# Performance work log

Measured on AMD Instinct MI355X. Metric: run time of the kernel, lower is better.

## Reference

```python
import jax, jax.numpy as jnp
import numpy as np

B, T, D_IN, D_H, D_OUT = 32, 1024, 512, 1024, 512

def setup_inputs() -> dict:
    key = jax.random.key(0)
    kx, k1, k2, k3, k4, k5, k6 = jax.random.split(key, 7)
    # scale weights like typical init (1/sqrt(fan_in)) so sigmoid stays in a sane range
    x = jax.random.normal(kx, (B, T, D_IN), dtype=jnp.float32)
    Wh_w = jax.random.normal(k1, (D_H, D_H), dtype=jnp.float32) / np.sqrt(D_H)
    Wh_b = jax.random.normal(k2, (D_H,), dtype=jnp.float32) * 0.01
    Wx_w = jax.random.normal(k3, (D_H, D_IN), dtype=jnp.float32) / np.sqrt(D_IN)
    Wx_b = jax.random.normal(k4, (D_H,), dtype=jnp.float32) * 0.01
    Wy_w = jax.random.normal(k5, (D_OUT, D_H), dtype=jnp.float32) / np.sqrt(D_H)
    Wy_b = jax.random.normal(k6, (D_OUT,), dtype=jnp.float32) * 0.01
    return {"x": x, "Wh_w": Wh_w, "Wh_b": Wh_b, "Wx_w": Wx_w, "Wx_b": Wx_b,
            "Wy_w": Wy_w, "Wy_b": Wy_b}

def reference(x, Wh_w, Wh_b, Wx_w, Wx_b, Wy_w, Wy_b):
    # h_t = sigmoid(Wh h_{t-1} + b_h + Wx x_t + b_x); y_t = Wy h_t + b_y
    # Precompute input projection for all timesteps (one big GEMM).
    xp = jnp.einsum('bti,hi->bth', x, Wx_w) + Wx_b + Wh_b  # [B,T,H]
    xp_t = jnp.swapaxes(xp, 0, 1)  # [T,B,H] for scan
    h0 = jnp.zeros((x.shape[0], Wh_w.shape[0]), dtype=x.dtype)

    def step(h, xpt):
        h = jax.nn.sigmoid(h @ Wh_w.T + xpt)  # [B,H]
        y = h @ Wy_w.T + Wy_b                 # [B,O]
        return h, y

    _, ys = jax.lax.scan(step, h0, xp_t)  # ys: [T,B,O]
    return jnp.swapaxes(ys, 0, 1)  # [B,T,O]
```

## Files before the change

kernel.cpp:

```cpp
#include <hip/hip_runtime.h>

constexpr int Bb = 32;
constexpr int Tt = 1024;
constexpr int Hh = 1024;
constexpr int Di = 512;
constexpr int Do = 512;
constexpr int TGSZ = Bb * Hh;

using bf16x8 = __attribute__((ext_vector_type(8))) short;
using f32x4  = __attribute__((ext_vector_type(4))) float;

__device__ __forceinline__ f32x4 mfma16(bf16x8 a, bf16x8 b, f32x4 c) {
  return __builtin_amdgcn_mfma_f32_16x16x32_bf16(a, b, c, 0, 0, 0);
}
__device__ __forceinline__ unsigned short f2bf(float f) {
  unsigned u = __builtin_bit_cast(unsigned, f);
  u += 0x7FFFu + ((u >> 16) & 1u);
  return (unsigned short)(u >> 16);
}
__device__ __forceinline__ float bf2f(unsigned short h) {
  unsigned u = ((unsigned)h) << 16;
  return __builtin_bit_cast(float, u);
}

__global__ __launch_bounds__(256) void cvt4_kernel(const float* __restrict__ s,
                                                   unsigned short* __restrict__ d) {
  int i = (blockIdx.x * 256 + threadIdx.x) * 4;
  float4 v = *(const float4*)(s + i);
  ushort4 u = { f2bf(v.x), f2bf(v.y), f2bf(v.z), f2bf(v.w) };
  *(ushort4*)(d + i) = u;
}

__global__ __launch_bounds__(256) void init_tags(unsigned* __restrict__ tg) {
  int i = blockIdx.x * 256 + threadIdx.x;
  tg[i] = (i < TGSZ) ? 0xFFFF0000u : 0xEEEE0000u;
}

template <int MODE>
__global__ __launch_bounds__(256)
void gemm_kernel(const void* __restrict__ Ap, const float* __restrict__ Bw,
                 const float* __restrict__ bias1, const float* __restrict__ bias2,
                 void* __restrict__ Cp) {
  constexpr int K = (MODE == 0) ? Di : Hh;
  constexpr int BM = 64, BN = 64, BK = 64;
  __shared__ unsigned short As[BM][80];
  __shared__ unsigned short Bs[BN][80];

  const int m0 = blockIdx.x * BM;
  const int n0 = blockIdx.y * BN;
  const int tid = threadIdx.x;
  const int lane = tid & 63;
  const int wave = tid >> 6;
  const int wm = (wave & 1) * 32;
  const int wn = (wave >> 1) * 32;
  const int fr = lane & 15;
  const int kg = lane >> 4;

  f32x4 acc[2][2] = {};

  const int srow = tid >> 2;
  const int scb  = (tid & 3) * 16;

  for (int k0 = 0; k0 < K; k0 += BK) {
    if constexpr (MODE == 0) {
      const float* a = (const float*)Ap + (size_t)(m0 + srow) * K + k0 + scb;
#pragma unroll
      for (int q = 0; q < 4; ++q) {
        float4 v = ((const float4*)a)[q];
        ushort4 u = { f2bf(v.x), f2bf(v.y), f2bf(v.z), f2bf(v.w) };
        *(ushort4*)&As[srow][scb + q * 4] = u;
      }
    } else {
      const unsigned short* a = (const unsigned short*)Ap + (size_t)(m0 + srow) * K + k0 + scb;
      *(uint4*)&As[srow][scb]     = ((const uint4*)a)[0];
      *(uint4*)&As[srow][scb + 8] = ((const uint4*)a)[1];
    }
    {
      const float* b = Bw + (size_t)(n0 + srow) * K + k0 + scb;
#pragma unroll
      for (int q = 0; q < 4; ++q) {
        float4 v = ((const float4*)b)[q];
        ushort4 u = { f2bf(v.x), f2bf(v.y), f2bf(v.z), f2bf(v.w) };
        *(ushort4*)&Bs[srow][scb + q * 4] = u;
      }
    }
    __syncthreads();

#pragma unroll
    for (int kk = 0; kk < 2; ++kk) {
      const int kb = kk * 32 + kg * 8;
      bf16x8 af[2], bfr[2];
      af[0]  = *(const bf16x8*)&As[wm + fr][kb];
      af[1]  = *(const bf16x8*)&As[wm + 16 + fr][kb];
      bfr[0] = *(const bf16x8*)&Bs[wn + fr][kb];
      bfr[1] = *(const bf16x8*)&Bs[wn + 16 + fr][kb];
#pragma unroll
      for (int i = 0; i < 2; ++i)
#pragma unroll
        for (int j = 0; j < 2; ++j)
          acc[i][j] = mfma16(af[i], bfr[j], acc[i][j]);
    }
    __syncthreads();
  }

#pragma unroll
  for (int i = 0; i < 2; ++i) {
#pragma unroll
    for (int j = 0; j < 2; ++j) {
      const int n = n0 + wn + j * 16 + fr;
      float bv;
      if constexpr (MODE == 0) bv = bias1[n] + bias2[n];
      else                     bv = bias1[n];
#pragma unroll
      for (int q = 0; q < 4; ++q) {
        const int m = m0 + wm + i * 16 + kg * 4 + q;
        float v = acc[i][j][q] + bv;
        if constexpr (MODE == 0) {
          int bb = m >> 10, ttt = m & 1023;
          ((unsigned short*)Cp)[((size_t)ttt * Bb + bb) * Hh + n] = f2bf(v);
        } else {
          int bb = m & 31, ttt = m >> 5;
          ((float*)Cp)[((size_t)bb * Tt + ttt) * Do + n] = v;
        }
      }
    }
  }
}

__global__ __launch_bounds__(512, 2)
void scan_kernel(const unsigned short* __restrict__ Whb,
                 const unsigned short* __restrict__ xp,
                 unsigned short* __restrict__ hist,
                 unsigned* __restrict__ tg) {
  __shared__ unsigned short panel[16 * 1024];

  const int tid = threadIdx.x;
  const int g = blockIdx.x >> 3;
  const int r = blockIdx.x & 7;
  const int wave = tid >> 6;
  const int lane = tid & 63;
  const int nloc = lane & 15;
  const int kgrp = lane >> 4;
  const int hrow = r * 128 + wave * 16 + nloc;
  const int gb0 = g * 16;
  const int xmask = (nloc & 7) << 3;

  bf16x8 wf[32];
  {
    const unsigned short* wb = Whb + (size_t)hrow * Hh + kgrp * 8;
#pragma unroll
    for (int kk = 0; kk < 32; kk += 8) {
      const unsigned short* p = wb + kk * 32;
      asm volatile(
          "global_load_dwordx4 %0, %8, off\n\t"
          "global_load_dwordx4 %1, %8, off offset:64\n\t"
          "global_load_dwordx4 %2, %8, off offset:128\n\t"
          "global_load_dwordx4 %3, %8, off offset:192\n\t"
          "global_load_dwordx4 %4, %8, off offset:256\n\t"
          "global_load_dwordx4 %5, %8, off offset:320\n\t"
          "global_load_dwordx4 %6, %8, off offset:384\n\t"
          "global_load_dwordx4 %7, %8, off offset:448\n\t"
          "s_waitcnt vmcnt(0)"
          : "=&v"(wf[kk + 0]), "=&v"(wf[kk + 1]), "=&v"(wf[kk + 2]), "=&v"(wf[kk + 3]),
            "=&v"(wf[kk + 4]), "=&v"(wf[kk + 5]), "=&v"(wf[kk + 6]), "=&v"(wf[kk + 7])
          : "v"(p)
          : "memory");
    }
  }

  const int sb  = tid & 15;
  const int kc  = tid >> 4;
  const int sxs = (sb & 7) << 3;

  for (int t = 0; t < Tt; ++t) {
    const int par = t % 3;
    const int nxt = (t + 1) % 3;

    unsigned short xpv[4];
    const size_t xb = (size_t)t * Bb * Hh + hrow;
#pragma unroll
    for (int i = 0; i < 4; ++i) xpv[i] = xp[xb + (size_t)(gb0 + kgrp * 4 + i) * Hh];

    const unsigned exp = ((unsigned)t - 1u) & 0xFFFFu;
    const unsigned* src = tg + (size_t)par * TGSZ + (size_t)(gb0 + sb) * Hh + kc * 32;
    uint4 d0, d1, d2, d3, d4, d5, d6, d7;
    unsigned bad;
    int tries = 8192;
    do {
      asm volatile(
          "global_load_dwordx4 %0, %8, off sc0 sc1\n\t"
          "global_load_dwordx4 %1, %8, off offset:16 sc0 sc1\n\t"
          "global_load_dwordx4 %2, %8, off offset:32 sc0 sc1\n\t"
          "global_load_dwordx4 %3, %8, off offset:48 sc0 sc1\n\t"
          "global_load_dwordx4 %4, %8, off offset:64 sc0 sc1\n\t"
          "global_load_dwordx4 %5, %8, off offset:80 sc0 sc1\n\t"
          "global_load_dwordx4 %6, %8, off offset:96 sc0 sc1\n\t"
          "global_load_dwordx4 %7, %8, off offset:112 sc0 sc1\n\t"
          "s_waitcnt vmcnt(0)"
          : "=&v"(d0), "=&v"(d1), "=&v"(d2), "=&v"(d3),
            "=&v"(d4), "=&v"(d5), "=&v"(d6), "=&v"(d7)
          : "v"(src) : "memory");
      bad = 0;
#define CHK(v) bad |= ((v.x >> 16) ^ exp) | ((v.y >> 16) ^ exp) | \
                      ((v.z >> 16) ^ exp) | ((v.w >> 16) ^ exp)
      CHK(d0); CHK(d1); CHK(d2); CHK(d3); CHK(d4); CHK(d5); CHK(d6); CHK(d7);
#undef CHK
    } while (bad && --tries);

    {
#define PK(a, b) (((a) & 0xFFFFu) | ((b) << 16))
      uint4 p0 = { PK(d0.x, d0.y), PK(d0.z, d0.w), PK(d1.x, d1.y), PK(d1.z, d1.w) };
      uint4 p1 = { PK(d2.x, d2.y), PK(d2.z, d2.w), PK(d3.x, d3.y), PK(d3.z, d3.w) };
      uint4 p2 = { PK(d4.x, d4.y), PK(d4.z, d4.w), PK(d5.x, d5.y), PK(d5.z, d5.w) };
      uint4 p3 = { PK(d6.x, d6.y), PK(d6.z, d6.w), PK(d7.x, d7.y), PK(d7.z, d7.w) };
#undef PK
      const int pb = sb * 1024, k0 = kc * 32;
      *(uint4*)&panel[pb + ((k0)      ^ sxs)] = p0;
      *(uint4*)&panel[pb + ((k0 + 8)  ^ sxs)] = p1;
      *(uint4*)&panel[pb + ((k0 + 16) ^ sxs)] = p2;
      *(uint4*)&panel[pb + ((k0 + 24) ^ sxs)] = p3;
    }
    __syncthreads();

    f32x4 acc0 = {0.f, 0.f, 0.f, 0.f}, acc1 = {0.f, 0.f, 0.f, 0.f};
#pragma unroll
    for (int kk = 0; kk < 32; kk += 2) {
      bf16x8 a0 = *(const bf16x8*)&panel[nloc * 1024 + ((kk * 32 + kgrp * 8) ^ xmask)];
      bf16x8 a1 = *(const bf16x8*)&panel[nloc * 1024 + (((kk + 1) * 32 + kgrp * 8) ^ xmask)];
      acc0 = mfma16(a0, wf[kk], acc0);
      acc1 = mfma16(a1, wf[kk + 1], acc1);
    }
    f32x4 acc = acc0 + acc1;

    const size_t tb = (size_t)t * Bb * Hh;
    unsigned* dbase = tg + (size_t)nxt * TGSZ + hrow;
#pragma unroll
    for (int i = 0; i < 4; ++i) {
      const int mb = gb0 + kgrp * 4 + i;
      float pre = acc[i] + bf2f(xpv[i]);
      float h = 1.0f / (1.0f + __expf(-pre));
      unsigned short hb = f2bf(h);
      unsigned word = ((unsigned)t << 16) | (unsigned)hb;
      asm volatile("global_store_dword %0, %1, off sc0 sc1"
                   :: "v"(dbase + (size_t)mb * Hh), "v"(word) : "memory");
      hist[tb + (size_t)mb * Hh + hrow] = hb;
    }

    __syncthreads();
  }
}

extern "C" void kernel_launch(void* const* d_in, const int* in_sizes, int n_in,
                              void* d_out, int out_size, void* d_ws, size_t ws_size,
                              hipStream_t stream) {
  const float* x    = (const float*)d_in[0];
  const float* Wh_w = (const float*)d_in[1];
  const float* Wh_b = (const float*)d_in[2];
  const float* Wx_w = (const float*)d_in[3];
  const float* Wx_b = (const float*)d_in[4];
  const float* Wy_w = (const float*)d_in[5];
  const float* Wy_b = (const float*)d_in[6];

  char* ws = (char*)d_ws;
  constexpr size_t XP_OFF   = 0;
  constexpr size_t HIST_OFF = XP_OFF   + (size_t)Tt * Bb * Hh * 2;
  constexpr size_t WH_OFF   = HIST_OFF + (size_t)Tt * Bb * Hh * 2;
  constexpr size_t TG_OFF   = WH_OFF   + (size_t)Hh * Hh * 2;

  unsigned short* xp   = (unsigned short*)(ws + XP_OFF);
  unsigned short* hist = (unsigned short*)(ws + HIST_OFF);
  unsigned short* whb  = (unsigned short*)(ws + WH_OFF);
  unsigned*       tg   = (unsigned*)(ws + TG_OFF);

  init_tags<<<dim3((3 * TGSZ) / 256), dim3(256), 0, stream>>>(tg);

  cvt4_kernel<<<dim3((Hh * Hh) / (256 * 4)), dim3(256), 0, stream>>>(Wh_w, whb);

  gemm_kernel<0><<<dim3((Bb * Tt) / 64, Hh / 64), dim3(256), 0, stream>>>(
      (const void*)x, Wx_w, Wx_b, Wh_b, (void*)xp);

  {
    void* sargs[4] = { (void*)&whb, (void*)&xp, (void*)&hist, (void*)&tg };
    hipLaunchCooperativeKernel((const void*)scan_kernel, dim3(16), dim3(512), sargs, 0, stream);
  }

  gemm_kernel<1><<<dim3((Bb * Tt) / 64, Do / 64), dim3(256), 0, stream>>>(
      (const void*)hist, Wy_w, Wy_b, nullptr, d_out);
}
```

Before: 5.856 ms.

## Replace tagged-word handoff with per-wave flags and direct global h loads

The scan's inter-block communication changes from 32-bit tagged words (value plus timestep), polled and repacked into LDS, to a double-buffered bf16 hidden-state array plus per-wave progress flags. Each wave polls 64 flags, then streams its A operand directly from global memory with pipelined loads interleaved with MFMAs, and needs no __syncthreads. The grid moves from 16 blocks of 512 threads to 32 blocks of 256, so more CUs take part. The aim is to halve handoff traffic and cut block-wide barriers from the per-step critical path, at the cost of redundant global reads of h per wave and a separate flag store after a full vmcnt wait.

```diff
diff --git a/kernel.cpp b/kernel.cpp
--- a/kernel.cpp
+++ b/kernel.cpp
@@ -5,7 +5,7 @@
 constexpr int Hh = 1024;
 constexpr int Di = 512;
 constexpr int Do = 512;
-constexpr int TGSZ = Bb * Hh;
+constexpr int BbHh = Bb * Hh;
 
 using bf16x8 = __attribute__((ext_vector_type(8))) short;
 using f32x4  = __attribute__((ext_vector_type(4))) float;
@@ -29,11 +29,6 @@
   float4 v = *(const float4*)(s + i);
   ushort4 u = { f2bf(v.x), f2bf(v.y), f2bf(v.z), f2bf(v.w) };
   *(ushort4*)(d + i) = u;
-}
-
-__global__ __launch_bounds__(256) void init_tags(unsigned* __restrict__ tg) {
-  int i = blockIdx.x * 256 + threadIdx.x;
-  tg[i] = (i < TGSZ) ? 0xFFFF0000u : 0xEEEE0000u;
 }
 
 template <int MODE>
@@ -127,23 +122,22 @@
   }
 }
 
-__global__ __launch_bounds__(512, 2)
+__global__ __launch_bounds__(256, 1)
 void scan_kernel(const unsigned short* __restrict__ Whb,
                  const unsigned short* __restrict__ xp,
                  unsigned short* __restrict__ hist,
-                 unsigned* __restrict__ tg) {
-  __shared__ unsigned short panel[16 * 1024];
-
+                 unsigned short* __restrict__ hbuf,
+                 unsigned* __restrict__ flags) {
   const int tid = threadIdx.x;
-  const int g = blockIdx.x >> 3;
-  const int r = blockIdx.x & 7;
+  const int g = blockIdx.x >> 4;
+  const int r = blockIdx.x & 15;
   const int wave = tid >> 6;
   const int lane = tid & 63;
   const int nloc = lane & 15;
   const int kgrp = lane >> 4;
-  const int hrow = r * 128 + wave * 16 + nloc;
+  const int W = r * 4 + wave;
+  const int hrow = W * 16 + nloc;
   const int gb0 = g * 16;
-  const int xmask = (nloc & 7) << 3;
 
   bf16x8 wf[32];
   {
@@ -168,85 +162,87 @@
     }
   }
 
-  const int sb  = tid & 15;
-  const int kc  = tid >> 4;
-  const int sxs = (sb & 7) << 3;
+  unsigned* fbase = flags + g * 64;
+  const unsigned* fp = fbase + lane;
 
   for (int t = 0; t < Tt; ++t) {
-    const int par = t % 3;
-    const int nxt = (t + 1) % 3;
+    const unsigned short* hrd = hbuf + (size_t)(t & 1) * BbHh;
+    unsigned short* hwr = hbuf + (size_t)((t + 1) & 1) * BbHh;
 
     unsigned short xpv[4];
-    const size_t xb = (size_t)t * Bb * Hh + hrow;
+    const size_t xb = (size_t)t * BbHh + hrow;
 #pragma unroll
     for (int i = 0; i < 4; ++i) xpv[i] = xp[xb + (size_t)(gb0 + kgrp * 4 + i) * Hh];
 
-    const unsigned exp = ((unsigned)t - 1u) & 0xFFFFu;
-    const unsigned* src = tg + (size_t)par * TGSZ + (size_t)(gb0 + sb) * Hh + kc * 32;
-    uint4 d0, d1, d2, d3, d4, d5, d6, d7;
-    unsigned bad;
-    int tries = 8192;
-    do {
-      asm volatile(
-          "global_load_dwordx4 %0, %8, off sc0 sc1\n\t"
-          "global_load_dwordx4 %1, %8, off offset:16 sc0 sc1\n\t"
-          "global_load_dwordx4 %2, %8, off offset:32 sc0 sc1\n\t"
-          "global_load_dwordx4 %3, %8, off offset:48 sc0 sc1\n\t"
-          "global_load_dwordx4 %4, %8, off offset:64 sc0 sc1\n\t"
-          "global_load_dwordx4 %5, %8, off offset:80 sc0 sc1\n\t"
-          "global_load_dwordx4 %6, %8, off offset:96 sc0 sc1\n\t"
-          "global_load_dwordx4 %7, %8, off offset:112 sc0 sc1\n\t"
-          "s_waitcnt vmcnt(0)"
-          : "=&v"(d0), "=&v"(d1), "=&v"(d2), "=&v"(d3),
-            "=&v"(d4), "=&v"(d5), "=&v"(d6), "=&v"(d7)
-          : "v"(src) : "memory");
-      bad = 0;
-#define CHK(v) bad |= ((v.x >> 16) ^ exp) | ((v.y >> 16) ^ exp) | \
-                      ((v.z >> 16) ^ exp) | ((v.w >> 16) ^ exp)
-      CHK(d0); CHK(d1); CHK(d2); CHK(d3); CHK(d4); CHK(d5); CHK(d6); CHK(d7);
-#undef CHK
-    } while (bad && --tries);
-
     {
-#define PK(a, b) (((a) & 0xFFFFu) | ((b) << 16))
-      uint4 p0 = { PK(d0.x, d0.y), PK(d0.z, d0.w), PK(d1.x, d1.y), PK(d1.z, d1.w) };
-      uint4 p1 = { PK(d2.x, d2.y), PK(d2.z, d2.w), PK(d3.x, d3.y), PK(d3.z, d3.w) };
-      uint4 p2 = { PK(d4.x, d4.y), PK(d4.z, d4.w), PK(d5.x, d5.y), PK(d5.z, d5.w) };
-      uint4 p3 = { PK(d6.x, d6.y), PK(d6.z, d6.w), PK(d7.x, d7.y), PK(d7.z, d7.w) };
-#undef PK
-      const int pb = sb * 1024, k0 = kc * 32;
-      *(uint4*)&panel[pb + ((k0)      ^ sxs)] = p0;
-      *(uint4*)&panel[pb + ((k0 + 8)  ^ sxs)] = p1;
-      *(uint4*)&panel[pb + ((k0 + 16) ^ sxs)] = p2;
-      *(uint4*)&panel[pb + ((k0 + 24) ^ sxs)] = p3;
-    }
-    __syncthreads();
-
+      unsigned fl;
+      int tries = 4096;
+      do {
+        asm volatile("global_load_dword %0, %1, off sc0 sc1\n\ts_waitcnt vmcnt(0)"
+                     : "=&v"(fl) : "v"(fp) : "memory");
+      } while (__any(fl < (unsigned)t) && --tries);
+    }
+
+    const unsigned short* abase = hrd + (size_t)(gb0 + nloc) * Hh + kgrp * 8;
     f32x4 acc0 = {0.f, 0.f, 0.f, 0.f}, acc1 = {0.f, 0.f, 0.f, 0.f};
-#pragma unroll
-    for (int kk = 0; kk < 32; kk += 2) {
-      bf16x8 a0 = *(const bf16x8*)&panel[nloc * 1024 + ((kk * 32 + kgrp * 8) ^ xmask)];
-      bf16x8 a1 = *(const bf16x8*)&panel[nloc * 1024 + (((kk + 1) * 32 + kgrp * 8) ^ xmask)];
-      acc0 = mfma16(a0, wf[kk], acc0);
-      acc1 = mfma16(a1, wf[kk + 1], acc1);
-    }
-    f32x4 acc = acc0 + acc1;
-
-    const size_t tb = (size_t)t * Bb * Hh;
-    unsigned* dbase = tg + (size_t)nxt * TGSZ + hrow;
+    f32x4 acc2 = {0.f, 0.f, 0.f, 0.f}, acc3 = {0.f, 0.f, 0.f, 0.f};
+    uint4 pa[16];
+
+#define ISSUE4(I, O0, O1, O2, O3)                                             \
+    asm volatile(                                                             \
+        "global_load_dwordx4 %0, %4, off offset:" #O0 " sc0 sc1\n\t"          \
+        "global_load_dwordx4 %1, %4, off offset:" #O1 " sc0 sc1\n\t"          \
+        "global_load_dwordx4 %2, %4, off offset:" #O2 " sc0 sc1\n\t"          \
+        "global_load_dwordx4 %3, %4, off offset:" #O3 " sc0 sc1"              \
+        : "=&v"(pa[I]), "=&v"(pa[I + 1]), "=&v"(pa[I + 2]), "=&v"(pa[I + 3])  \
+        : "v"(abase) : "memory")
+
+#define CONSUME4(I, KB, N)                                                    \
+    asm volatile("s_waitcnt vmcnt(" #N ")" ::: "memory");                     \
+    __builtin_amdgcn_sched_barrier(0);                                        \
+    acc0 = mfma16(__builtin_bit_cast(bf16x8, pa[I]),     wf[KB],     acc0);   \
+    acc1 = mfma16(__builtin_bit_cast(bf16x8, pa[I + 1]), wf[KB + 1], acc1);   \
+    acc2 = mfma16(__builtin_bit_cast(bf16x8, pa[I + 2]), wf[KB + 2], acc2);   \
+    acc3 = mfma16(__builtin_bit_cast(bf16x8, pa[I + 3]), wf[KB + 3], acc3);   \
+    __builtin_amdgcn_sched_barrier(0)
+
+    ISSUE4(0,    0,   64,  128,  192);
+    ISSUE4(4,  256,  320,  384,  448);
+    ISSUE4(8,  512,  576,  640,  704);
+    ISSUE4(12, 768,  832,  896,  960);
+    CONSUME4(0,  0, 12);
+    CONSUME4(4,  4,  8);
+    CONSUME4(8,  8,  4);
+    CONSUME4(12, 12, 0);
+
+    ISSUE4(0,  1024, 1088, 1152, 1216);
+    ISSUE4(4,  1280, 1344, 1408, 1472);
+    ISSUE4(8,  1536, 1600, 1664, 1728);
+    ISSUE4(12, 1792, 1856, 1920, 1984);
+    CONSUME4(0,  16, 12);
+    CONSUME4(4,  20,  8);
+    CONSUME4(8,  24,  4);
+    CONSUME4(12, 28, 0);
+#undef ISSUE4
+#undef CONSUME4
+    f32x4 acc = (acc0 + acc1) + (acc2 + acc3);
+
+    const size_t tb = (size_t)t * BbHh;
 #pragma unroll
     for (int i = 0; i < 4; ++i) {
       const int mb = gb0 + kgrp * 4 + i;
       float pre = acc[i] + bf2f(xpv[i]);
       float h = 1.0f / (1.0f + __expf(-pre));
       unsigned short hb = f2bf(h);
-      unsigned word = ((unsigned)t << 16) | (unsigned)hb;
+      asm volatile("global_store_short %0, %1, off sc0 sc1"
+                   :: "v"(hwr + (size_t)mb * Hh + hrow), "v"((unsigned)hb) : "memory");
+      hist[tb + (size_t)mb * Hh + hrow] = hb;
+    }
+
+    asm volatile("s_waitcnt vmcnt(0)" ::: "memory");
+    if (lane == 0)
       asm volatile("global_store_dword %0, %1, off sc0 sc1"
-                   :: "v"(dbase + (size_t)mb * Hh), "v"(word) : "memory");
-      hist[tb + (size_t)mb * Hh + hrow] = hb;
-    }
-
-    __syncthreads();
+                   :: "v"(fbase + W), "v"((unsigned)(t + 1)) : "memory");
   }
 }
 
@@ -265,14 +261,16 @@
   constexpr size_t XP_OFF   = 0;
   constexpr size_t HIST_OFF = XP_OFF   + (size_t)Tt * Bb * Hh * 2;
   constexpr size_t WH_OFF   = HIST_OFF + (size_t)Tt * Bb * Hh * 2;
-  constexpr size_t TG_OFF   = WH_OFF   + (size_t)Hh * Hh * 2;
-
-  unsigned short* xp   = (unsigned short*)(ws + XP_OFF);
-  unsigned short* hist = (unsigned short*)(ws + HIST_OFF);
-  unsigned short* whb  = (unsigned short*)(ws + WH_OFF);
-  unsigned*       tg   = (unsigned*)(ws + TG_OFF);
-
-  init_tags<<<dim3((3 * TGSZ) / 256), dim3(256), 0, stream>>>(tg);
+  constexpr size_t HBUF_OFF = WH_OFF   + (size_t)Hh * Hh * 2;
+  constexpr size_t FLG_OFF  = HBUF_OFF + (size_t)2 * BbHh * 2;
+
+  unsigned short* xp    = (unsigned short*)(ws + XP_OFF);
+  unsigned short* hist  = (unsigned short*)(ws + HIST_OFF);
+  unsigned short* whb   = (unsigned short*)(ws + WH_OFF);
+  unsigned short* hbuf  = (unsigned short*)(ws + HBUF_OFF);
+  unsigned*       flags = (unsigned*)(ws + FLG_OFF);
+
+  hipMemsetAsync(ws + HBUF_OFF, 0, (size_t)2 * BbHh * 2 + 512, stream);
 
   cvt4_kernel<<<dim3((Hh * Hh) / (256 * 4)), dim3(256), 0, stream>>>(Wh_w, whb);
 
@@ -280,8 +278,12 @@
       (const void*)x, Wx_w, Wx_b, Wh_b, (void*)xp);
 
   {
-    void* sargs[4] = { (void*)&whb, (void*)&xp, (void*)&hist, (void*)&tg };
-    hipLaunchCooperativeKernel((const void*)scan_kernel, dim3(16), dim3(512), sargs, 0, stream);
+    void* sargs[5] = { (void*)&whb, (void*)&xp, (void*)&hist, (void*)&hbuf, (void*)&flags };
+    hipError_t ce = hipLaunchCooperativeKernel((const void*)scan_kernel, dim3(32), dim3(256),
+                                               sargs, 0, stream);
+    if (ce != hipSuccess) {
+      scan_kernel<<<dim3(32), dim3(256), 0, stream>>>(whb, xp, hist, hbuf, flags);
+    }
   }
 
   gemm_kernel<1><<<dim3((Bb * Tt) / 64, Do / 64), dim3(256), 0, stream>>>(
```

Measured after the change: 8.078 ms. 1.38x slower.
